# Optimization experiments

Measured on AMD Instinct MI355X. Metric: run time of the kernel, lower is better.

The kernel has to match this reference:

```python
import jax, jax.numpy as jnp
import numpy as np

EPS = 1e-6
NH, D_NOPE, D_ROPE, DV = 16, 128, 64, 128
DQK = D_NOPE + D_ROPE  # 192
KV_LORA = 512
Q_LORA = 1536
TOP_K, N_GROUP, TOPK_GROUP, N_EXP = 2, 4, 2, 8
INTER = 768
SCALING = DQK ** -0.5  # rope_scaling is None -> no yarn mscale
RSF = 2.5  # routed_scaling_factor


def rms_norm(x, w):
    v = jnp.mean(jnp.square(x), axis=-1, keepdims=True)
    return x * jax.lax.rsqrt(v + EPS) * w


def rotate_half(x):
    x1, x2 = jnp.split(x, 2, axis=-1)
    return jnp.concatenate([-x2, x1], axis=-1)


def interleave(x):
    # view(b,h,s,d//2,2).transpose(4,3).reshape(b,h,s,d): evens then odds
    b, h, s, d = x.shape
    return x.reshape(b, h, s, d // 2, 2).swapaxes(-1, -2).reshape(b, h, s, d)


def mlp(x, gw, uw, dw):
    return (jax.nn.silu(x @ gw.T) * (x @ uw.T)) @ dw.T


def setup_inputs() -> dict:
    key = jax.random.key(0)
    ks = jax.random.split(key, 16)
    B, S, H = 2, 1024, 2048
    sd = 0.02

    def p(k, shape):
        return jax.random.normal(k, shape, jnp.float32) * sd

    # standard RoPE cos/sin table
    inv_freq = 1.0 / (10000.0 ** (jnp.arange(0, D_ROPE, 2, dtype=jnp.float32) / D_ROPE))
    pos = jnp.arange(S, dtype=jnp.float32)
    freqs = pos[:, None] * inv_freq[None, :]
    emb = jnp.concatenate([freqs, freqs], axis=-1)  # [S, D_ROPE]
    cos = jnp.broadcast_to(jnp.cos(emb)[None], (B, S, D_ROPE))
    sin = jnp.broadcast_to(jnp.sin(emb)[None], (B, S, D_ROPE))

    return dict(
        hidden_states=jax.random.normal(ks[0], (B, S, H), jnp.float32),
        cos=cos,
        sin=sin,
        ln1_w=jnp.ones((H,), jnp.float32),
        q_a_w=p(ks[1], (Q_LORA, H)),
        q_a_ln_w=jnp.ones((Q_LORA,), jnp.float32),
        q_b_w=p(ks[2], (NH * DQK, Q_LORA)),
        kv_a_w=p(ks[3], (KV_LORA + D_ROPE, H)),
        kv_a_ln_w=jnp.ones((KV_LORA,), jnp.float32),
        kv_b_w=p(ks[4], (NH * (D_NOPE + DV), KV_LORA)),
        o_w=p(ks[5], (H, NH * DV)),
        ln2_w=jnp.ones((H,), jnp.float32),
        router_w=p(ks[6], (N_EXP, H)),
        router_bias=jnp.zeros((N_EXP,), jnp.float32),
        gate_w=p(ks[7], (N_EXP, INTER, H)),
        up_w=p(ks[8], (N_EXP, INTER, H)),
        down_w=p(ks[9], (N_EXP, H, INTER)),
        sh_gate_w=p(ks[10], (INTER, H)),
        sh_up_w=p(ks[11], (INTER, H)),
        sh_down_w=p(ks[12], (H, INTER)),
    )


def reference(hidden_states, cos, sin, ln1_w, q_a_w, q_a_ln_w, q_b_w, kv_a_w,
              kv_a_ln_w, kv_b_w, o_w, ln2_w, router_w, router_bias,
              gate_w, up_w, down_w, sh_gate_w, sh_up_w, sh_down_w):
    B, S, H = hidden_states.shape
    # ----- input_layernorm + MLA attention -----
    resid = hidden_states
    x = rms_norm(hidden_states, ln1_w)

    q = rms_norm(x @ q_a_w.T, q_a_ln_w) @ q_b_w.T       # [B,S,NH*DQK]
    q = q.reshape(B, S, NH, DQK).transpose(0, 2, 1, 3)   # [B,NH,S,DQK]
    q_pass, q_rot = q[..., :D_NOPE], q[..., D_NOPE:]

    ckv = x @ kv_a_w.T                                   # [B,S,KV_LORA+D_ROPE]
    k_pass_c, k_rot = ckv[..., :KV_LORA], ckv[..., KV_LORA:]
    kv = rms_norm(k_pass_c, kv_a_ln_w) @ kv_b_w.T        # [B,S,NH*(D_NOPE+DV)]
    kv = kv.reshape(B, S, NH, D_NOPE + DV).transpose(0, 2, 1, 3)
    k_pass, v = kv[..., :D_NOPE], kv[..., D_NOPE:]

    k_rot = k_rot.reshape(B, 1, S, D_ROPE)
    c = cos[:, None]  # [B,1,S,D_ROPE]
    s_ = sin[:, None]
    q_rot = interleave(q_rot)
    k_rot = interleave(k_rot)
    q_rot = q_rot * c + rotate_half(q_rot) * s_
    k_rot = k_rot * c + rotate_half(k_rot) * s_
    k_rot = jnp.broadcast_to(k_rot, (B, NH, S, D_ROPE))

    qs = jnp.concatenate([q_pass, q_rot], axis=-1)       # [B,NH,S,DQK]
    ks = jnp.concatenate([k_pass, k_rot], axis=-1)

    scores = jnp.einsum('bhqd,bhkd->bhqk', qs, ks) * SCALING
    causal = jnp.tril(jnp.ones((S, S), dtype=bool))
    scores = jnp.where(causal, scores, -jnp.inf)
    probs = jax.nn.softmax(scores, axis=-1)
    attn = jnp.einsum('bhqk,bhkd->bhqd', probs, v)
    attn = attn.transpose(0, 2, 1, 3).reshape(B, S, NH * DV)
    x = resid + attn @ o_w.T

    # ----- post_attention_layernorm + MoE -----
    resid = x
    h = rms_norm(x, ln2_w)
    t = h.reshape(-1, H)

    # router (fp32)
    scores_r = jax.nn.sigmoid(t.astype(jnp.float32) @ router_w.T.astype(jnp.float32))
    sc = scores_r + router_bias[None, :]
    gs = sc.reshape(-1, N_GROUP, N_EXP // N_GROUP)
    group_scores = jax.lax.top_k(gs, 2)[0].sum(-1)          # [T,G]
    gidx = jax.lax.top_k(group_scores, TOPK_GROUP)[1]
    gmask = jax.nn.one_hot(gidx, N_GROUP).sum(1)            # [T,G]
    emask = jnp.repeat(gmask, N_EXP // N_GROUP, axis=-1)    # [T,E]
    masked = jnp.where(emask > 0, sc, 0.0)
    idx = jax.lax.top_k(masked, TOP_K)[1]                   # [T,k]
    w = jnp.take_along_axis(scores_r, idx, axis=-1)
    w = w / (w.sum(-1, keepdims=True) + 1e-20) * RSF

    # routed experts: dense-all-experts compute, then routed-weight combine
    gate_h = jnp.einsum('td,eid->tei', t, gate_w)
    up_h = jnp.einsum('td,eid->tei', t, up_w)
    eo = jnp.einsum('tei,edi->ted', jax.nn.silu(gate_h) * up_h, down_w)
    dense_w = (jax.nn.one_hot(idx, N_EXP) * w[..., None]).sum(1)  # [T,E]
    moe_out = jnp.einsum('ted,te->td', eo, dense_w).reshape(B, S, H)

    shared = mlp(h, sh_gate_w, sh_up_w, sh_down_w)
    return resid + moe_out + shared
```

## Files before the change

kernel.cpp:

```cpp
#include <hip/hip_runtime.h>

typedef float f4 __attribute__((ext_vector_type(4)));
typedef float f32x4 __attribute__((ext_vector_type(4)));
typedef unsigned short us8 __attribute__((ext_vector_type(8)));
typedef __bf16 bf8 __attribute__((ext_vector_type(8)));

static constexpr int B_ = 2, S_ = 1024, H_ = 2048, T_ = B_ * S_;
static constexpr int NH_ = 16, DN_ = 128, DR_ = 64, DV_ = 128, DQK_ = 192;
static constexpr int KVL_ = 512, QL_ = 1536, INTER_ = 768, NEXP_ = 8, NE9_ = 9;
static constexpr int QKA_ = 2176;
static constexpr float SCALING_ = 0.07216878364870322f;
static constexpr float EPS_ = 1e-6f;

__device__ __forceinline__ unsigned short f2bf(float f) {
    unsigned u = __float_as_uint(f);
    u += 0x7fffu + ((u >> 16) & 1u);
    return (unsigned short)(u >> 16);
}
__device__ __forceinline__ float bf2f(unsigned short h) {
    return __uint_as_float(((unsigned)h) << 16);
}
__device__ __forceinline__ us8 pack8(f4 a, f4 b) {
    us8 r;
    r[0] = f2bf(a[0]); r[1] = f2bf(a[1]); r[2] = f2bf(a[2]); r[3] = f2bf(a[3]);
    r[4] = f2bf(b[0]); r[5] = f2bf(b[1]); r[6] = f2bf(b[2]); r[7] = f2bf(b[3]);
    return r;
}

__device__ __forceinline__ void gload16(const unsigned short* g, unsigned short* lds) {
    __builtin_amdgcn_global_load_lds(
        (const __attribute__((address_space(1))) void*)g,
        (__attribute__((address_space(3))) void*)lds, 16, 0, 0);
}

template <int MODE>
__global__ __launch_bounds__(256) void gemm2(
    const unsigned short* __restrict__ A, const unsigned short* __restrict__ Bw,
    float* __restrict__ Cf, unsigned short* __restrict__ Cb,
    const float* __restrict__ add,
    const int* __restrict__ cnt, const int* __restrict__ off,
    const int* __restrict__ idxl, const float* __restrict__ wl,
    int M, int N, int K, int ldA, long sB)
{
    constexpr int BM = 128, BN = 128, BK = 64;
    __shared__ __align__(16) unsigned short As[2][BM * BK];
    __shared__ __align__(16) unsigned short Bs[2][BN * BK];
    const int tid = threadIdx.x, lane = tid & 63, wv = tid >> 6;
    const int wm = (wv >> 1) * 64, wn = (wv & 1) * 64;

    const int nb = gridDim.x * gridDim.y;
    const int lin = blockIdx.y * gridDim.x + blockIdx.x;
    const int swz = (lin & 7) * (nb >> 3) + (lin >> 3);
    const int bx = swz % gridDim.x;
    const int by = swz / gridDim.x;
    const int m0 = bx * BM, n0 = by * BN;

    int mcnt = M, obase = 0;
    if constexpr (MODE != 0) {
        mcnt = cnt[blockIdx.z];
        if (m0 >= mcnt) return;
        obase = off[blockIdx.z];
    }

    const int srow = tid >> 3;
    const int scol = (((tid & 7) ^ (srow & 7)) * 8);
    long aoff[4], boff[4];
#pragma unroll
    for (int s = 0; s < 4; s++) {
        int r = m0 + s * 32 + srow;
        if constexpr (MODE == 1) {
            int rc = (r < mcnt) ? r : mcnt - 1;
            aoff[s] = (long)idxl[(long)blockIdx.z * T_ + rc] * ldA + scol;
        } else if constexpr (MODE == 2) {
            aoff[s] = (long)(obase + r) * ldA + scol;
        } else {
            aoff[s] = (long)r * ldA + scol;
        }
        boff[s] = (long)blockIdx.z * sB + (long)(n0 + s * 32 + srow) * K + scol;
    }

    f32x4 acc[4][4];
#pragma unroll
    for (int m = 0; m < 4; m++)
#pragma unroll
        for (int n = 0; n < 4; n++) acc[m][n] = f32x4{0.f, 0.f, 0.f, 0.f};

    const int fr = lane & 15, lg = lane >> 4;
    const int xr = fr & 7;

    auto stage = [&](int buf, int k0) {
#pragma unroll
        for (int s = 0; s < 4; s++)
            gload16(A + aoff[s] + k0, &As[buf][s * 2048 + wv * 512]);
#pragma unroll
        for (int s = 0; s < 4; s++)
            gload16(Bw + boff[s] + k0, &Bs[buf][s * 2048 + wv * 512]);
    };
    auto compute = [&](int buf) {
        __builtin_amdgcn_s_setprio(1);
        bf8 af[4][2], bfv[4][2];
#pragma unroll
        for (int m = 0; m < 4; m++) {
            int R = wm + m * 16 + fr;
#pragma unroll
            for (int ks = 0; ks < 2; ks++)
                af[m][ks] = *(const bf8*)&As[buf][R * 64 + ((ks * 4 + lg) ^ xr) * 8];
        }
#pragma unroll
        for (int n = 0; n < 4; n++) {
            int R = wn + n * 16 + fr;
#pragma unroll
            for (int ks = 0; ks < 2; ks++)
                bfv[n][ks] = *(const bf8*)&Bs[buf][R * 64 + ((ks * 4 + lg) ^ xr) * 8];
        }
#pragma unroll
        for (int m = 0; m < 4; m++)
#pragma unroll
            for (int n = 0; n < 4; n++) {
                acc[m][n] = __builtin_amdgcn_mfma_f32_16x16x32_bf16(af[m][0], bfv[n][0], acc[m][n], 0, 0, 0);
                acc[m][n] = __builtin_amdgcn_mfma_f32_16x16x32_bf16(af[m][1], bfv[n][1], acc[m][n], 0, 0, 0);
            }
        __builtin_amdgcn_s_setprio(0);
    };

    const int nt = K / BK;
    stage(0, 0);
    for (int t = 0; t < nt; t++) {
        if (t + 1 < nt) {
            stage((t & 1) ^ 1, (t + 1) * BK);
            asm volatile("s_waitcnt vmcnt(8)" ::: "memory");
        } else {
            asm volatile("s_waitcnt vmcnt(0)" ::: "memory");
        }
        __builtin_amdgcn_s_barrier();
        compute(t & 1);
        __builtin_amdgcn_s_barrier();
    }

#pragma unroll
    for (int m = 0; m < 4; m++) {
#pragma unroll
        for (int n = 0; n < 4; n++) {
#pragma unroll
            for (int i = 0; i < 4; i++) {
                int row = wm + m * 16 + (lane >> 4) * 4 + i;
                int col = n0 + wn + n * 16 + (lane & 15);
                float v = acc[m][n][i];
                if constexpr (MODE == 0) {
                    long idx = (long)(m0 + row) * N + col;
                    if (Cb)       Cb[idx] = f2bf(v);
                    else if (add) Cf[idx] = v + add[idx];
                    else          Cf[idx] = v;
                } else if constexpr (MODE == 1) {
                    if (m0 + row < mcnt)
                        Cb[(long)(obase + m0 + row) * N + col] = f2bf(v);
                } else {
                    if (m0 + row < mcnt) {
                        int e = blockIdx.z;
                        int tok = idxl[(long)e * T_ + m0 + row];
                        float w = wl[(long)e * T_ + m0 + row];
                        atomicAdd(&Cf[(long)tok * N + col], w * v);
                    }
                }
            }
        }
    }
}

__global__ __launch_bounds__(256) void fa_k(
    const unsigned short* __restrict__ qs, const unsigned short* __restrict__ ks,
    const unsigned short* __restrict__ vt, unsigned short* __restrict__ ab)
{
    constexpr int KB = 64;
    const int q0 = blockIdx.x * 64;
    const int bh = blockIdx.y;
    const int b = bh >> 4, h = bh & 15;
    const int tid = threadIdx.x, lane = tid & 63, wv = tid >> 6;
    const int fr = lane & 15, lg = lane >> 4;
    const int ko = lg * 8;

    __shared__ __align__(16) unsigned short Kl[KB][200];
    __shared__ __align__(16) unsigned short Vl[128][72];
    __shared__ __align__(16) unsigned short Pl[4][16][72];

    const unsigned short* qp = qs + ((long)bh * S_ + q0 + wv * 16 + fr) * DQK_ + ko;
    bf8 qf[6];
#pragma unroll
    for (int s = 0; s < 6; s++) qf[s] = *(const bf8*)(qp + s * 32);

    f32x4 o[8];
#pragma unroll
    for (int n = 0; n < 8; n++) o[n] = f32x4{0.f, 0.f, 0.f, 0.f};
    float mrow[4] = {-3e38f, -3e38f, -3e38f, -3e38f};
    float lrow[4] = {0.f, 0.f, 0.f, 0.f};

    const int nt = q0 / KB + 1;

    const unsigned short* kg = ks + ((long)bh * S_ + (tid >> 2)) * DQK_ + (tid & 3) * 48;
    const unsigned short* vg = vt + ((long)bh * DV_ + (tid >> 1)) * S_ + (tid & 1) * 32;

    us8 krg[6], vrg[4];
#pragma unroll
    for (int j = 0; j < 6; j++) krg[j] = *(const us8*)(kg + j * 8);
#pragma unroll
    for (int j = 0; j < 4; j++) vrg[j] = *(const us8*)(vg + j * 8);

    for (int t = 0; t < nt; t++) {
        __syncthreads();
        {
            int r = tid >> 2, c = (tid & 3) * 48;
#pragma unroll
            for (int j = 0; j < 6; j++) *(us8*)&Kl[r][c + j * 8] = krg[j];
            int dv = tid >> 1, c2 = (tid & 1) * 32;
#pragma unroll
            for (int j = 0; j < 4; j++) *(us8*)&Vl[dv][c2 + j * 8] = vrg[j];
        }
        __syncthreads();
        if (t + 1 < nt) {
            long kof = (long)(t + 1) * KB;
#pragma unroll
            for (int j = 0; j < 6; j++) krg[j] = *(const us8*)(kg + kof * DQK_ + j * 8);
#pragma unroll
            for (int j = 0; j < 4; j++) vrg[j] = *(const us8*)(vg + kof + j * 8);
        }
        f32x4 ps[4];
#pragma unroll
        for (int ct = 0; ct < 4; ct++) {
            f32x4 a = f32x4{0.f, 0.f, 0.f, 0.f};
#pragma unroll
            for (int s = 0; s < 6; s++) {
                bf8 kf = *(const bf8*)&Kl[ct * 16 + fr][s * 32 + ko];
                a = __builtin_amdgcn_mfma_f32_16x16x32_bf16(qf[s], kf, a, 0, 0, 0);
            }
            ps[ct] = a;
        }
        const int kv0 = t * KB;
        const bool diag = (kv0 == q0);
#pragma unroll
        for (int ct = 0; ct < 4; ct++)
#pragma unroll
            for (int i = 0; i < 4; i++) {
                float v = ps[ct][i] * SCALING_;
                if (diag && (kv0 + ct * 16 + fr) > (q0 + wv * 16 + lg * 4 + i)) v = -3e38f;
                ps[ct][i] = v;
            }
        float scl[4];
#pragma unroll
        for (int i = 0; i < 4; i++) {
            float v = fmaxf(fmaxf(ps[0][i], ps[1][i]), fmaxf(ps[2][i], ps[3][i]));
#pragma unroll
            for (int x = 8; x; x >>= 1) v = fmaxf(v, __shfl_xor(v, x, 16));
            float mn = fmaxf(mrow[i], v);
            scl[i] = __expf(mrow[i] - mn);
            mrow[i] = mn;
        }
        float tsum[4] = {0.f, 0.f, 0.f, 0.f};
#pragma unroll
        for (int ct = 0; ct < 4; ct++)
#pragma unroll
            for (int i = 0; i < 4; i++) {
                float e = __expf(ps[ct][i] - mrow[i]);
                tsum[i] += e;
                Pl[wv][lg * 4 + i][ct * 16 + fr] = f2bf(e);
            }
#pragma unroll
        for (int i = 0; i < 4; i++) {
            float v = tsum[i];
#pragma unroll
            for (int x = 8; x; x >>= 1) v += __shfl_xor(v, x, 16);
            lrow[i] = lrow[i] * scl[i] + v;
        }
#pragma unroll
        for (int n = 0; n < 8; n++)
#pragma unroll
            for (int i = 0; i < 4; i++) o[n][i] *= scl[i];
        bf8 pf[2];
#pragma unroll
        for (int ksl = 0; ksl < 2; ksl++)
            pf[ksl] = *(const bf8*)&Pl[wv][fr][ksl * 32 + ko];
#pragma unroll
        for (int n = 0; n < 8; n++)
#pragma unroll
            for (int ksl = 0; ksl < 2; ksl++) {
                bf8 vf = *(const bf8*)&Vl[n * 16 + fr][ksl * 32 + ko];
                o[n] = __builtin_amdgcn_mfma_f32_16x16x32_bf16(pf[ksl], vf, o[n], 0, 0, 0);
            }
    }
#pragma unroll
    for (int i = 0; i < 4; i++) {
        float inv = 1.f / lrow[i];
        long rbase = ((long)b * S_ + q0 + wv * 16 + lg * 4 + i) * H_ + h * DV_;
#pragma unroll
        for (int n = 0; n < 8; n++)
            ab[rbase + n * 16 + fr] = f2bf(o[n][i] * inv);
    }
}

__global__ __launch_bounds__(256) void cvt_k(
    const float* __restrict__ s, unsigned short* __restrict__ d, long n)
{
    long i = ((long)blockIdx.x * 256 + threadIdx.x) * 8;
    if (i < n) {
        f4 a = *(const f4*)(s + i);
        f4 b = *(const f4*)(s + i + 4);
        *(us8*)(d + i) = pack8(a, b);
    }
}

__global__ __launch_bounds__(256) void cvt_qka_k(
    const float* __restrict__ qa, const float* __restrict__ kva,
    unsigned short* __restrict__ d)
{
    long i = ((long)blockIdx.x * 256 + threadIdx.x) * 8;
    long row = i >> 11, col = i & 2047;
    us8 o;
    if (row < QL_) {
        const float* s = qa + row * H_ + col;
        o = pack8(*(const f4*)s, *(const f4*)(s + 4));
    } else if (row < QL_ + 576) {
        const float* s = kva + (row - QL_) * H_ + col;
        o = pack8(*(const f4*)s, *(const f4*)(s + 4));
    } else {
        o = us8{0, 0, 0, 0, 0, 0, 0, 0};
    }
    *(us8*)(d + i) = o;
}

__global__ __launch_bounds__(256) void cvt_cat9_k(
    const float* __restrict__ g, const float* __restrict__ u,
    const float* __restrict__ sg, const float* __restrict__ su,
    unsigned short* __restrict__ d)
{
    long ii = ((long)blockIdx.x * 256 + threadIdx.x) * 8;
    int e = blockIdx.y;
    long row = ii >> 11, col = ii & 2047;
    const float* src;
    if (row < INTER_)
        src = (e < 8) ? (g + ((long)e * INTER_ + row) * H_ + col) : (sg + row * H_ + col);
    else
        src = (e < 8) ? (u + ((long)e * INTER_ + row - INTER_) * H_ + col)
                      : (su + (row - INTER_) * H_ + col);
    *(us8*)(d + (long)e * (2 * INTER_) * H_ + ii) = pack8(*(const f4*)src, *(const f4*)(src + 4));
}

__global__ __launch_bounds__(256) void rmsnorm_f2b(
    const float* __restrict__ in, const float* __restrict__ w,
    unsigned short* __restrict__ ob, float* __restrict__ of)
{
    const long base = (long)blockIdx.x * H_;
    const int c = threadIdx.x * 8;
    f4 v0 = *(const f4*)(in + base + c);
    f4 v1 = *(const f4*)(in + base + c + 4);
    float ss = v0[0] * v0[0] + v0[1] * v0[1] + v0[2] * v0[2] + v0[3] * v0[3]
             + v1[0] * v1[0] + v1[1] * v1[1] + v1[2] * v1[2] + v1[3] * v1[3];
#pragma unroll
    for (int o = 32; o; o >>= 1) ss += __shfl_down(ss, o);
    __shared__ float red[4];
    if ((threadIdx.x & 63) == 0) red[threadIdx.x >> 6] = ss;
    __syncthreads();
    float r = rsqrtf((red[0] + red[1] + red[2] + red[3]) / H_ + EPS_);
    f4 w0 = *(const f4*)(w + c);
    f4 w1 = *(const f4*)(w + c + 4);
    f4 a, b;
#pragma unroll
    for (int j = 0; j < 4; j++) { a[j] = v0[j] * r * w0[j]; b[j] = v1[j] * r * w1[j]; }
    *(us8*)(ob + base + c) = pack8(a, b);
    if (of) {
        *(f4*)(of + base + c) = a;
        *(f4*)(of + base + c + 4) = b;
    }
}

__global__ __launch_bounds__(256) void rmsnorm_b2b(
    const unsigned short* __restrict__ in, const float* __restrict__ w,
    unsigned short* __restrict__ out, int cols, int istride, int ostride)
{
    const long ib = (long)blockIdx.x * istride;
    const long ob = (long)blockIdx.x * ostride;
    const int nu = cols >> 3;
    float ss = 0.f;
    for (int u = threadIdx.x; u < nu; u += 256) {
        us8 v = *(const us8*)(in + ib + u * 8);
#pragma unroll
        for (int j = 0; j < 8; j++) { float f = bf2f(v[j]); ss += f * f; }
    }
#pragma unroll
    for (int o = 32; o; o >>= 1) ss += __shfl_down(ss, o);
    __shared__ float red[4];
    if ((threadIdx.x & 63) == 0) red[threadIdx.x >> 6] = ss;
    __syncthreads();
    float r = rsqrtf((red[0] + red[1] + red[2] + red[3]) / cols + EPS_);
    for (int u = threadIdx.x; u < nu; u += 256) {
        us8 v = *(const us8*)(in + ib + u * 8);
        f4 w0 = *(const f4*)(w + u * 8);
        f4 w1 = *(const f4*)(w + u * 8 + 4);
        us8 o;
#pragma unroll
        for (int j = 0; j < 4; j++) o[j] = f2bf(bf2f(v[j]) * r * w0[j]);
#pragma unroll
        for (int j = 0; j < 4; j++) o[4 + j] = f2bf(bf2f(v[4 + j]) * r * w1[j]);
        *(us8*)(out + ob + u * 8) = o;
    }
}

__global__ __launch_bounds__(64) void rope_q_k(
    const unsigned short* __restrict__ q, const float* __restrict__ cs,
    const float* __restrict__ sn, unsigned short* __restrict__ qs)
{
    int t = blockIdx.x;
    int h = t & 15;
    int bs = t >> 4;
    int s = bs & (S_ - 1);
    int b = bs >> 10;
    const unsigned short* qrow = q + (long)bs * (NH_ * DQK_) + h * DQK_;
    unsigned short* orow = qs + ((long)(b * NH_ + h) * S_ + s) * DQK_;
    int l = threadIdx.x;
    orow[l] = qrow[l];
    orow[l + 64] = qrow[l + 64];
    int j = l & 31;
    float x0 = bf2f(qrow[DN_ + 2 * j]), x1 = bf2f(qrow[DN_ + 2 * j + 1]);
    float c = cs[(long)bs * DR_ + j], si = sn[(long)bs * DR_ + j];
    if (l < 32) orow[DN_ + j] = f2bf(x0 * c - x1 * si);
    else        orow[DN_ + 32 + j] = f2bf(x1 * c + x0 * si);
}

__global__ __launch_bounds__(64) void rope_k_k(
    const unsigned short* __restrict__ qkab, const float* __restrict__ cs,
    const float* __restrict__ sn, unsigned short* __restrict__ ks)
{
    int bs = blockIdx.x;
    int s = bs & (S_ - 1);
    int b = bs >> 10;
    const unsigned short* kr = qkab + (long)bs * QKA_ + QL_ + KVL_;
    int l = threadIdx.x;
    int j = l & 31;
    float x0 = bf2f(kr[2 * j]), x1 = bf2f(kr[2 * j + 1]);
    float c = cs[(long)bs * DR_ + j], si = sn[(long)bs * DR_ + j];
    float val = (l < 32) ? (x0 * c - x1 * si) : (x1 * c + x0 * si);
    int off = (l < 32) ? (DN_ + j) : (DN_ + 32 + j);
    unsigned short bv = f2bf(val);
    for (int h = 0; h < NH_; h++)
        ks[((long)(b * NH_ + h) * S_ + s) * DQK_ + off] = bv;
}

__global__ __launch_bounds__(128) void kpass_k(
    const unsigned short* __restrict__ kv, unsigned short* __restrict__ ks)
{
    int t = blockIdx.x;
    int h = t & 15;
    int bs = t >> 4;
    int s = bs & (S_ - 1);
    int b = bs >> 10;
    ks[((long)(b * NH_ + h) * S_ + s) * DQK_ + threadIdx.x] = kv[(long)t * 256 + threadIdx.x];
}

__global__ __launch_bounds__(256) void vt_k(
    const unsigned short* __restrict__ kv, unsigned short* __restrict__ vt)
{
    __shared__ unsigned short tile[64][DV_ + 8];
    int s0 = blockIdx.x * 64;
    int bh = blockIdx.y;
    int b = bh >> 4, h = bh & 15;
#pragma unroll
    for (int it = 0; it < 4; it++) {
        int idx = it * 256 + threadIdx.x;
        int sl = idx >> 4, du = idx & 15;
        *(us8*)&tile[sl][du * 8] =
            *(const us8*)(kv + ((long)(b * S_ + s0 + sl) * NH_ + h) * 256 + DN_ + du * 8);
    }
    __syncthreads();
#pragma unroll
    for (int it = 0; it < 4; it++) {
        int idx = it * 256 + threadIdx.x;
        int d = idx >> 3, su = idx & 7;
        us8 o;
#pragma unroll
        for (int j = 0; j < 8; j++) o[j] = tile[su * 8 + j][d];
        *(us8*)(vt + ((long)bh * DV_ + d) * S_ + s0 + su * 8) = o;
    }
}

__global__ void zero9_k(int* __restrict__ cnt)
{
    if (threadIdx.x < NE9_) cnt[threadIdx.x] = (threadIdx.x == 8) ? T_ : 0;
}

__global__ void offs_k(const int* __restrict__ cnt, int* __restrict__ off)
{
    if (threadIdx.x == 0) {
        int a = 0;
        for (int e = 0; e < NE9_; e++) { off[e] = a; a += cnt[e]; }
    }
}

__global__ __launch_bounds__(64) void router_k(
    const float* __restrict__ h, const float* __restrict__ rw,
    const float* __restrict__ rb, int* __restrict__ cnt,
    int* __restrict__ idxl, float* __restrict__ wl)
{
    int t = blockIdx.x;
    int l = threadIdx.x;
    const float* hr = h + (long)t * H_;
    float pe[8] = {0, 0, 0, 0, 0, 0, 0, 0};
    for (int k = l; k < H_; k += 64) {
        float hv = hr[k];
#pragma unroll
        for (int e = 0; e < 8; e++) pe[e] += hv * rw[e * H_ + k];
    }
#pragma unroll
    for (int e = 0; e < 8; e++)
        for (int o = 32; o; o >>= 1) pe[e] += __shfl_down(pe[e], o);
    if (l == 0) {
        float sr[8], sc[8];
#pragma unroll
        for (int e = 0; e < 8; e++) {
            sr[e] = 1.f / (1.f + __expf(-pe[e]));
            sc[e] = sr[e] + rb[e];
        }
        float gs[4];
        for (int g = 0; g < 4; g++) gs[g] = sc[2 * g] + sc[2 * g + 1];
        int g0 = 0;
        for (int g = 1; g < 4; g++) if (gs[g] > gs[g0]) g0 = g;
        int g1 = -1;
        for (int g = 0; g < 4; g++) {
            if (g == g0) continue;
            if (g1 < 0 || gs[g] > gs[g1]) g1 = g;
        }
        int i0 = -1, i1 = -1;
        for (int e = 0; e < 8; e++) {
            int g = e >> 1;
            if (g != g0 && g != g1) continue;
            if (i0 < 0 || sc[e] > sc[i0]) i0 = e;
        }
        for (int e = 0; e < 8; e++) {
            int g = e >> 1;
            if (g != g0 && g != g1) continue;
            if (e == i0) continue;
            if (i1 < 0 || sc[e] > sc[i1]) i1 = e;
        }
        float w0 = sr[i0], w1 = sr[i1];
        float inv = 2.5f / (w0 + w1 + 1e-20f);
        int p0 = atomicAdd(&cnt[i0], 1);
        idxl[i0 * T_ + p0] = t;
        wl[i0 * T_ + p0] = w0 * inv;
        int p1 = atomicAdd(&cnt[i1], 1);
        idxl[i1 * T_ + p1] = t;
        wl[i1 * T_ + p1] = w1 * inv;
        idxl[8 * T_ + t] = t;
        wl[8 * T_ + t] = 1.0f;
    }
}

__global__ __launch_bounds__(256) void silugu_k(
    const unsigned short* __restrict__ gu, unsigned short* __restrict__ act)
{
    long idx = (long)blockIdx.x * 256 + threadIdx.x;
    int r = (int)(idx / 96);
    int c = (int)(idx - (long)r * 96) * 8;
    us8 g8 = *(const us8*)(gu + (long)r * (2 * INTER_) + c);
    us8 u8 = *(const us8*)(gu + (long)r * (2 * INTER_) + INTER_ + c);
    us8 o;
#pragma unroll
    for (int j = 0; j < 8; j++) {
        float g = bf2f(g8[j]);
        o[j] = f2bf(g / (1.f + __expf(-g)) * bf2f(u8[j]));
    }
    *(us8*)(act + (long)r * INTER_ + c) = o;
}

extern "C" void kernel_launch(void* const* d_in, const int* in_sizes, int n_in,
                              void* d_out, int out_size, void* d_ws, size_t ws_size,
                              hipStream_t stream)
{
    const float* hidden = (const float*)d_in[0];
    const float* cosb   = (const float*)d_in[1];
    const float* sinb   = (const float*)d_in[2];
    const float* ln1w   = (const float*)d_in[3];
    const float* qaw    = (const float*)d_in[4];
    const float* qalnw  = (const float*)d_in[5];
    const float* qbw    = (const float*)d_in[6];
    const float* kvaw   = (const float*)d_in[7];
    const float* kvalnw = (const float*)d_in[8];
    const float* kvbw   = (const float*)d_in[9];
    const float* ow     = (const float*)d_in[10];
    const float* ln2w   = (const float*)d_in[11];
    const float* rw     = (const float*)d_in[12];
    const float* rb     = (const float*)d_in[13];
    const float* gw     = (const float*)d_in[14];
    const float* uw     = (const float*)d_in[15];
    const float* dwn    = (const float*)d_in[16];
    const float* sgw    = (const float*)d_in[17];
    const float* suw    = (const float*)d_in[18];
    const float* sdw    = (const float*)d_in[19];
    float* out = (float*)d_out;
    (void)in_sizes; (void)n_in; (void)out_size; (void)ws_size;

    char* ws = (char*)d_ws;
    const size_t MB = 1u << 20;
    unsigned short* qkawb = (unsigned short*)(ws + 0 * MB);
    unsigned short* qbwb  = (unsigned short*)(ws + 9 * MB);
    unsigned short* kvbwb = (unsigned short*)(ws + 18 * MB);
    unsigned short* owb   = (unsigned short*)(ws + 22 * MB);
    unsigned short* xb    = (unsigned short*)(ws + 30 * MB);
    unsigned short* qkab  = (unsigned short*)(ws + 38 * MB);
    unsigned short* qb16  = (unsigned short*)(ws + 47 * MB);
    unsigned short* ckvnb = (unsigned short*)(ws + 59 * MB);
    unsigned short* kvb   = (unsigned short*)(ws + 61 * MB);
    unsigned short* qs    = (unsigned short*)(ws + 77 * MB);
    unsigned short* ks    = (unsigned short*)(ws + 89 * MB);
    unsigned short* vt    = (unsigned short*)(ws + 30 * MB);
    unsigned short* ab    = (unsigned short*)(ws + 38 * MB);
    float* hbuf = (float*)(ws + 0 * MB);
    unsigned short* actm = (unsigned short*)(ws + 0 * MB);
    unsigned short* hb16 = (unsigned short*)(ws + 16 * MB);
    int*   cnt  = (int*)(ws + 24 * MB);
    int*   offb = (int*)(ws + 24 * MB + 256);
    int*   idxl = (int*)(ws + 24 * MB + 512);
    float* wl   = (float*)(ws + 24 * MB + 512 + 9 * T_ * 4);
    unsigned short* guwb = (unsigned short*)(ws + 25 * MB);
    unsigned short* dwnb = (unsigned short*)(ws + 25 * MB);
    unsigned short* gu   = (unsigned short*)(ws + 79 * MB);

    cvt_qka_k<<<(QKA_ * H_) / 2048, 256, 0, stream>>>(qaw, kvaw, qkawb);
    cvt_k<<<(NH_ * DQK_ * QL_) / 2048, 256, 0, stream>>>(qbw, qbwb, (long)NH_ * DQK_ * QL_);
    cvt_k<<<(NH_ * 256 * KVL_) / 2048, 256, 0, stream>>>(kvbw, kvbwb, (long)NH_ * 256 * KVL_);
    cvt_k<<<(H_ * H_) / 2048, 256, 0, stream>>>(ow, owb, (long)H_ * H_);

    rmsnorm_f2b<<<T_, 256, 0, stream>>>(hidden, ln1w, xb, nullptr);

    gemm2<0><<<dim3(T_ / 128, QKA_ / 128, 1), 256, 0, stream>>>(
        xb, qkawb, nullptr, qkab, nullptr, nullptr, nullptr, nullptr, nullptr,
        T_, QKA_, H_, H_, 0);
    rmsnorm_b2b<<<T_, 256, 0, stream>>>(qkab, qalnw, qkab, QL_, QKA_, QKA_);
    gemm2<0><<<dim3(T_ / 128, (NH_ * DQK_) / 128, 1), 256, 0, stream>>>(
        qkab, qbwb, nullptr, qb16, nullptr, nullptr, nullptr, nullptr, nullptr,
        T_, NH_ * DQK_, QL_, QKA_, 0);
    rmsnorm_b2b<<<T_, 256, 0, stream>>>(qkab + QL_, kvalnw, ckvnb, KVL_, QKA_, KVL_);
    gemm2<0><<<dim3(T_ / 128, (NH_ * 256) / 128, 1), 256, 0, stream>>>(
        ckvnb, kvbwb, nullptr, kvb, nullptr, nullptr, nullptr, nullptr, nullptr,
        T_, NH_ * 256, KVL_, KVL_, 0);

    rope_q_k<<<T_ * NH_, 64, 0, stream>>>(qb16, cosb, sinb, qs);
    rope_k_k<<<T_, 64, 0, stream>>>(qkab, cosb, sinb, ks);
    kpass_k<<<T_ * NH_, 128, 0, stream>>>(kvb, ks);
    vt_k<<<dim3(S_ / 64, B_ * NH_), 256, 0, stream>>>(kvb, vt);

    fa_k<<<dim3(S_ / 64, B_ * NH_), 256, 0, stream>>>(qs, ks, vt, ab);

    gemm2<0><<<dim3(T_ / 128, H_ / 128, 1), 256, 0, stream>>>(
        ab, owb, out, nullptr, hidden, nullptr, nullptr, nullptr, nullptr,
        T_, H_, H_, H_, 0);

    rmsnorm_f2b<<<T_, 256, 0, stream>>>(out, ln2w, hb16, hbuf);
    zero9_k<<<1, 64, 0, stream>>>(cnt);
    router_k<<<T_, 64, 0, stream>>>(hbuf, rw, rb, cnt, idxl, wl);
    offs_k<<<1, 64, 0, stream>>>(cnt, offb);

    cvt_cat9_k<<<dim3((2 * INTER_ * H_) / 2048, NE9_), 256, 0, stream>>>(gw, uw, sgw, suw, guwb);
    gemm2<1><<<dim3(T_ / 128, (2 * INTER_) / 128, NE9_), 256, 0, stream>>>(
        hb16, guwb, nullptr, gu, nullptr, cnt, offb, idxl, nullptr,
        T_, 2 * INTER_, H_, H_, (long)(2 * INTER_) * H_);
    silugu_k<<<(3 * T_ * 96) / 256, 256, 0, stream>>>(gu, actm);
    cvt_k<<<(NEXP_ * H_ * INTER_) / 2048, 256, 0, stream>>>(dwn, dwnb, (long)NEXP_ * H_ * INTER_);
    cvt_k<<<(H_ * INTER_) / 2048, 256, 0, stream>>>(sdw, dwnb + (long)NEXP_ * H_ * INTER_, (long)H_ * INTER_);
    gemm2<2><<<dim3(T_ / 128, H_ / 128, NE9_), 256, 0, stream>>>(
        actm, dwnb, out, nullptr, nullptr, cnt, offb, idxl, wl,
        T_, H_, INTER_, INTER_, (long)H_ * INTER_);
}
```

Before: 534.4 us.

## Fuse SiLU into gate/up GEMM and replace atomic scatter with gather combine

```diff
diff --git a/kernel.cpp b/kernel.cpp
--- a/kernel.cpp
+++ b/kernel.cpp
@@ -39,7 +39,6 @@
     float* __restrict__ Cf, unsigned short* __restrict__ Cb,
     const float* __restrict__ add,
     const int* __restrict__ cnt, const int* __restrict__ off,
-    const int* __restrict__ idxl, const float* __restrict__ wl,
     int M, int N, int K, int ldA, long sB)
 {
     constexpr int BM = 128, BN = 128, BK = 64;
@@ -56,7 +55,7 @@
     const int m0 = bx * BM, n0 = by * BN;
 
     int mcnt = M, obase = 0;
-    if constexpr (MODE != 0) {
+    if constexpr (MODE == 2) {
         mcnt = cnt[blockIdx.z];
         if (m0 >= mcnt) return;
         obase = off[blockIdx.z];
@@ -68,10 +67,7 @@
 #pragma unroll
     for (int s = 0; s < 4; s++) {
         int r = m0 + s * 32 + srow;
-        if constexpr (MODE == 1) {
-            int rc = (r < mcnt) ? r : mcnt - 1;
-            aoff[s] = (long)idxl[(long)blockIdx.z * T_ + rc] * ldA + scol;
-        } else if constexpr (MODE == 2) {
+        if constexpr (MODE == 2) {
             aoff[s] = (long)(obase + r) * ldA + scol;
         } else {
             aoff[s] = (long)r * ldA + scol;
@@ -143,24 +139,136 @@
         for (int n = 0; n < 4; n++) {
 #pragma unroll
             for (int i = 0; i < 4; i++) {
-                int row = wm + m * 16 + (lane >> 4) * 4 + i;
-                int col = n0 + wn + n * 16 + (lane & 15);
+                int row = wm + m * 16 + lg * 4 + i;
+                int col = n0 + wn + n * 16 + fr;
                 float v = acc[m][n][i];
                 if constexpr (MODE == 0) {
                     long idx = (long)(m0 + row) * N + col;
                     if (Cb)       Cb[idx] = f2bf(v);
                     else if (add) Cf[idx] = v + add[idx];
                     else          Cf[idx] = v;
-                } else if constexpr (MODE == 1) {
+                } else {
                     if (m0 + row < mcnt)
                         Cb[(long)(obase + m0 + row) * N + col] = f2bf(v);
-                } else {
-                    if (m0 + row < mcnt) {
-                        int e = blockIdx.z;
-                        int tok = idxl[(long)e * T_ + m0 + row];
-                        float w = wl[(long)e * T_ + m0 + row];
-                        atomicAdd(&Cf[(long)tok * N + col], w * v);
-                    }
+                }
+            }
+        }
+    }
+}
+
+__global__ __launch_bounds__(256) void gemm_gu(
+    const unsigned short* __restrict__ A, const unsigned short* __restrict__ Bw,
+    unsigned short* __restrict__ actm,
+    const int* __restrict__ cnt, const int* __restrict__ off,
+    const int* __restrict__ idxl)
+{
+    constexpr int BM = 128, BN = 128, BK = 64, K = H_;
+    __shared__ __align__(16) unsigned short As[2][BM * BK];
+    __shared__ __align__(16) unsigned short Bg[2][BN * BK];
+    __shared__ __align__(16) unsigned short Bu[2][BN * BK];
+    const int tid = threadIdx.x, lane = tid & 63, wv = tid >> 6;
+    const int wm = (wv >> 1) * 64, wn = (wv & 1) * 64;
+
+    const int nb = gridDim.x * gridDim.y;
+    const int lin = blockIdx.y * gridDim.x + blockIdx.x;
+    const int swz = (lin & 7) * (nb >> 3) + (lin >> 3);
+    const int bx = swz % gridDim.x;
+    const int by = swz / gridDim.x;
+    const int m0 = bx * BM, n0 = by * BN;
+    const int e = blockIdx.z;
+
+    const int mcnt = cnt[e];
+    if (m0 >= mcnt) return;
+    const int obase = off[e];
+
+    const int srow = tid >> 3;
+    const int scol = (((tid & 7) ^ (srow & 7)) * 8);
+    long aoff[4], bgo[4], buo[4];
+#pragma unroll
+    for (int s = 0; s < 4; s++) {
+        int r = m0 + s * 32 + srow;
+        int rc = (r < mcnt) ? r : mcnt - 1;
+        aoff[s] = (long)idxl[(long)e * T_ + rc] * H_ + scol;
+        bgo[s] = ((long)e * (2 * INTER_) + n0 + s * 32 + srow) * K + scol;
+        buo[s] = ((long)e * (2 * INTER_) + INTER_ + n0 + s * 32 + srow) * K + scol;
+    }
+
+    f32x4 ag[4][4], au[4][4];
+#pragma unroll
+    for (int m = 0; m < 4; m++)
+#pragma unroll
+        for (int n = 0; n < 4; n++) {
+            ag[m][n] = f32x4{0.f, 0.f, 0.f, 0.f};
+            au[m][n] = f32x4{0.f, 0.f, 0.f, 0.f};
+        }
+
+    const int fr = lane & 15, lg = lane >> 4;
+    const int xr = fr & 7;
+
+    auto stage = [&](int buf, int k0) {
+#pragma unroll
+        for (int s = 0; s < 4; s++)
+            gload16(A + aoff[s] + k0, &As[buf][s * 2048 + wv * 512]);
+#pragma unroll
+        for (int s = 0; s < 4; s++)
+            gload16(Bw + bgo[s] + k0, &Bg[buf][s * 2048 + wv * 512]);
+#pragma unroll
+        for (int s = 0; s < 4; s++)
+            gload16(Bw + buo[s] + k0, &Bu[buf][s * 2048 + wv * 512]);
+    };
+    auto compute = [&](int buf) {
+        __builtin_amdgcn_s_setprio(1);
+        bf8 bgf[4][2], buf_[4][2];
+#pragma unroll
+        for (int n = 0; n < 4; n++) {
+            int R = wn + n * 16 + fr;
+#pragma unroll
+            for (int ks = 0; ks < 2; ks++) {
+                bgf[n][ks] = *(const bf8*)&Bg[buf][R * 64 + ((ks * 4 + lg) ^ xr) * 8];
+                buf_[n][ks] = *(const bf8*)&Bu[buf][R * 64 + ((ks * 4 + lg) ^ xr) * 8];
+            }
+        }
+#pragma unroll
+        for (int m = 0; m < 4; m++) {
+            int R = wm + m * 16 + fr;
+            bf8 a0 = *(const bf8*)&As[buf][R * 64 + ((0 + lg) ^ xr) * 8];
+            bf8 a1 = *(const bf8*)&As[buf][R * 64 + ((4 + lg) ^ xr) * 8];
+#pragma unroll
+            for (int n = 0; n < 4; n++) {
+                ag[m][n] = __builtin_amdgcn_mfma_f32_16x16x32_bf16(a0, bgf[n][0], ag[m][n], 0, 0, 0);
+                ag[m][n] = __builtin_amdgcn_mfma_f32_16x16x32_bf16(a1, bgf[n][1], ag[m][n], 0, 0, 0);
+                au[m][n] = __builtin_amdgcn_mfma_f32_16x16x32_bf16(a0, buf_[n][0], au[m][n], 0, 0, 0);
+                au[m][n] = __builtin_amdgcn_mfma_f32_16x16x32_bf16(a1, buf_[n][1], au[m][n], 0, 0, 0);
+            }
+        }
+        __builtin_amdgcn_s_setprio(0);
+    };
+
+    const int nt = K / BK;
+    stage(0, 0);
+    for (int t = 0; t < nt; t++) {
+        if (t + 1 < nt) {
+            stage((t & 1) ^ 1, (t + 1) * BK);
+            asm volatile("s_waitcnt vmcnt(12)" ::: "memory");
+        } else {
+            asm volatile("s_waitcnt vmcnt(0)" ::: "memory");
+        }
+        __builtin_amdgcn_s_barrier();
+        compute(t & 1);
+        __builtin_amdgcn_s_barrier();
+    }
+
+#pragma unroll
+    for (int m = 0; m < 4; m++) {
+#pragma unroll
+        for (int n = 0; n < 4; n++) {
+#pragma unroll
+            for (int i = 0; i < 4; i++) {
+                int row = wm + m * 16 + lg * 4 + i;
+                if (m0 + row < mcnt) {
+                    float g = ag[m][n][i], u = au[m][n][i];
+                    float v = g / (1.f + __expf(-g)) * u;
+                    actm[(long)(obase + m0 + row) * INTER_ + n0 + wn + n * 16 + fr] = f2bf(v);
                 }
             }
         }
@@ -496,7 +604,7 @@
 __global__ __launch_bounds__(64) void router_k(
     const float* __restrict__ h, const float* __restrict__ rw,
     const float* __restrict__ rb, int* __restrict__ cnt,
-    int* __restrict__ idxl, float* __restrict__ wl)
+    int* __restrict__ idxl, int* __restrict__ tep, float* __restrict__ tww)
 {
     int t = blockIdx.x;
     int l = threadIdx.x;
@@ -542,30 +650,34 @@
         float inv = 2.5f / (w0 + w1 + 1e-20f);
         int p0 = atomicAdd(&cnt[i0], 1);
         idxl[i0 * T_ + p0] = t;
-        wl[i0 * T_ + p0] = w0 * inv;
         int p1 = atomicAdd(&cnt[i1], 1);
         idxl[i1 * T_ + p1] = t;
-        wl[i1 * T_ + p1] = w1 * inv;
+        tep[t * 4 + 0] = i0; tep[t * 4 + 1] = p0;
+        tep[t * 4 + 2] = i1; tep[t * 4 + 3] = p1;
+        tww[t * 2 + 0] = w0 * inv;
+        tww[t * 2 + 1] = w1 * inv;
         idxl[8 * T_ + t] = t;
-        wl[8 * T_ + t] = 1.0f;
-    }
-}
-
-__global__ __launch_bounds__(256) void silugu_k(
-    const unsigned short* __restrict__ gu, unsigned short* __restrict__ act)
-{
-    long idx = (long)blockIdx.x * 256 + threadIdx.x;
-    int r = (int)(idx / 96);
-    int c = (int)(idx - (long)r * 96) * 8;
-    us8 g8 = *(const us8*)(gu + (long)r * (2 * INTER_) + c);
-    us8 u8 = *(const us8*)(gu + (long)r * (2 * INTER_) + INTER_ + c);
-    us8 o;
-#pragma unroll
-    for (int j = 0; j < 8; j++) {
-        float g = bf2f(g8[j]);
-        o[j] = f2bf(g / (1.f + __expf(-g)) * bf2f(u8[j]));
-    }
-    *(us8*)(act + (long)r * INTER_ + c) = o;
+    }
+}
+
+__global__ __launch_bounds__(256) void gather_k(
+    const unsigned short* __restrict__ pd, const int* __restrict__ off,
+    const int* __restrict__ tep, const float* __restrict__ tww,
+    float* __restrict__ out)
+{
+    int t = blockIdx.x;
+    int e0 = tep[t * 4], p0 = tep[t * 4 + 1];
+    int e1 = tep[t * 4 + 2], p1 = tep[t * 4 + 3];
+    float w0 = tww[t * 2], w1 = tww[t * 2 + 1];
+    long r0 = (long)(off[e0] + p0) * H_;
+    long r1 = (long)(off[e1] + p1) * H_;
+    int c = threadIdx.x * 8;
+    us8 a = *(const us8*)(pd + r0 + c);
+    us8 b = *(const us8*)(pd + r1 + c);
+    float* op = out + (long)t * H_ + c;
+#pragma unroll
+    for (int j = 0; j < 8; j++)
+        op[j] += w0 * bf2f(a[j]) + w1 * bf2f(b[j]);
 }
 
 extern "C" void kernel_launch(void* const* d_in, const int* in_sizes, int n_in,
@@ -616,10 +728,11 @@
     int*   cnt  = (int*)(ws + 24 * MB);
     int*   offb = (int*)(ws + 24 * MB + 256);
     int*   idxl = (int*)(ws + 24 * MB + 512);
-    float* wl   = (float*)(ws + 24 * MB + 512 + 9 * T_ * 4);
+    int*   tep  = (int*)(ws + 24 * MB + 512 + 9 * T_ * 4);
+    float* tww  = (float*)(ws + 24 * MB + 512 + 9 * T_ * 4 + 4 * T_ * 4);
     unsigned short* guwb = (unsigned short*)(ws + 25 * MB);
     unsigned short* dwnb = (unsigned short*)(ws + 25 * MB);
-    unsigned short* gu   = (unsigned short*)(ws + 79 * MB);
+    unsigned short* pd   = (unsigned short*)(ws + 79 * MB);
 
     cvt_qka_k<<<(QKA_ * H_) / 2048, 256, 0, stream>>>(qaw, kvaw, qkawb);
     cvt_k<<<(NH_ * DQK_ * QL_) / 2048, 256, 0, stream>>>(qbw, qbwb, (long)NH_ * DQK_ * QL_);
@@ -629,15 +742,15 @@
     rmsnorm_f2b<<<T_, 256, 0, stream>>>(hidden, ln1w, xb, nullptr);
 
     gemm2<0><<<dim3(T_ / 128, QKA_ / 128, 1), 256, 0, stream>>>(
-        xb, qkawb, nullptr, qkab, nullptr, nullptr, nullptr, nullptr, nullptr,
+        xb, qkawb, nullptr, qkab, nullptr, nullptr, nullptr,
         T_, QKA_, H_, H_, 0);
     rmsnorm_b2b<<<T_, 256, 0, stream>>>(qkab, qalnw, qkab, QL_, QKA_, QKA_);
     gemm2<0><<<dim3(T_ / 128, (NH_ * DQK_) / 128, 1), 256, 0, stream>>>(
-        qkab, qbwb, nullptr, qb16, nullptr, nullptr, nullptr, nullptr, nullptr,
+        qkab, qbwb, nullptr, qb16, nullptr, nullptr, nullptr,
         T_, NH_ * DQK_, QL_, QKA_, 0);
     rmsnorm_b2b<<<T_, 256, 0, stream>>>(qkab + QL_, kvalnw, ckvnb, KVL_, QKA_, KVL_);
     gemm2<0><<<dim3(T_ / 128, (NH_ * 256) / 128, 1), 256, 0, stream>>>(
-        ckvnb, kvbwb, nullptr, kvb, nullptr, nullptr, nullptr, nullptr, nullptr,
+        ckvnb, kvbwb, nullptr, kvb, nullptr, nullptr, nullptr,
         T_, NH_ * 256, KVL_, KVL_, 0);
 
     rope_q_k<<<T_ * NH_, 64, 0, stream>>>(qb16, cosb, sinb, qs);
@@ -648,22 +761,28 @@
     fa_k<<<dim3(S_ / 64, B_ * NH_), 256, 0, stream>>>(qs, ks, vt, ab);
 
     gemm2<0><<<dim3(T_ / 128, H_ / 128, 1), 256, 0, stream>>>(
-        ab, owb, out, nullptr, hidden, nullptr, nullptr, nullptr, nullptr,
+        ab, owb, out, nullptr, hidden, nullptr, nullptr,
         T_, H_, H_, H_, 0);
 
     rmsnorm_f2b<<<T_, 256, 0, stream>>>(out, ln2w, hb16, hbuf);
     zero9_k<<<1, 64, 0, stream>>>(cnt);
-    router_k<<<T_, 64, 0, stream>>>(hbuf, rw, rb, cnt, idxl, wl);
+    router_k<<<T_, 64, 0, stream>>>(hbuf, rw, rb, cnt, idxl, tep, tww);
     offs_k<<<1, 64, 0, stream>>>(cnt, offb);
 
     cvt_cat9_k<<<dim3((2 * INTER_ * H_) / 2048, NE9_), 256, 0, stream>>>(gw, uw, sgw, suw, guwb);
-    gemm2<1><<<dim3(T_ / 128, (2 * INTER_) / 128, NE9_), 256, 0, stream>>>(
-        hb16, guwb, nullptr, gu, nullptr, cnt, offb, idxl, nullptr,
-        T_, 2 * INTER_, H_, H_, (long)(2 * INTER_) * H_);
-    silugu_k<<<(3 * T_ * 96) / 256, 256, 0, stream>>>(gu, actm);
+    gemm_gu<<<dim3(T_ / 128, INTER_ / 128, NE9_), 256, 0, stream>>>(
+        hb16, guwb, actm, cnt, offb, idxl);
+
     cvt_k<<<(NEXP_ * H_ * INTER_) / 2048, 256, 0, stream>>>(dwn, dwnb, (long)NEXP_ * H_ * INTER_);
     cvt_k<<<(H_ * INTER_) / 2048, 256, 0, stream>>>(sdw, dwnb + (long)NEXP_ * H_ * INTER_, (long)H_ * INTER_);
-    gemm2<2><<<dim3(T_ / 128, H_ / 128, NE9_), 256, 0, stream>>>(
-        actm, dwnb, out, nullptr, nullptr, cnt, offb, idxl, wl,
+
+    gemm2<0><<<dim3(T_ / 128, H_ / 128, 1), 256, 0, stream>>>(
+        actm + (long)4096 * INTER_, dwnb + (long)NEXP_ * H_ * INTER_,
+        out, nullptr, out, nullptr, nullptr,
+        T_, H_, INTER_, INTER_, 0);
+
+    gemm2<2><<<dim3(T_ / 128, H_ / 128, NEXP_), 256, 0, stream>>>(
+        actm, dwnb, nullptr, pd, nullptr, cnt, offb,
         T_, H_, INTER_, INTER_, (long)H_ * INTER_);
-}
+    gather_k<<<T_, 256, 0, stream>>>(pd, offb, tep, tww, out);
+}
```

After: 555.8 us. 1.04x slower.
